# Kernel tuning notes

Hardware: AMD Instinct MI355X
Metric: run time of the kernel (lower is better)

Reference implementation:

```python
import jax, jax.numpy as jnp
import numpy as np

NUM_BITS = 4
N_VAL = 2 ** NUM_BITS - 1            # 15
INTERVAL = 2.0 / N_VAL               # init_range / n_val (non-trainable)
ZERO = 0.0                           # self.zero (non-trainable, default init)
EPS = 1e-3


def setup_inputs() -> dict:
    key = jax.random.key(0)
    k1, k2 = jax.random.split(key)
    x = jax.random.normal(k1, (32, 256, 56, 56), dtype=jnp.float32)
    # learned bin widths, initialized near `interval` with some spread
    a = (INTERVAL * (0.8 + 0.4 * jax.random.uniform(k2, (N_VAL,)))).astype(jnp.float32)
    start = jnp.full((1,), -1.0, dtype=jnp.float32)  # quantization range start
    scale1 = jnp.ones((1,), dtype=jnp.float32)
    scale2 = jnp.ones((1,), dtype=jnp.float32)
    return {"x": x, "start": start, "a": a, "scale1": scale1, "scale2": scale2}


def reference(x, start, a, scale1, scale2):
    xs = x * scale1                              # broadcast scalar
    s = start[0]
    a_pos = jnp.where(a > EPS, a, EPS)           # [n_val]
    cums = jnp.cumsum(a_pos)                     # [n_val]
    # thre_backward[i] = start + sum_{j<i} a_pos[j]
    tb = s + jnp.concatenate([jnp.zeros((1,), a_pos.dtype), cums[:-1]])
    # thre_forward[i] = thre_backward[i] + a_pos[i]/2
    tf = tb + a_pos * 0.5
    dt = xs.dtype

    # forward (hard) branch: count of strict exceedances of the sorted tf
    cnt_f = jnp.searchsorted(tf, xs, side="left")        # in [0, n_val]
    x_forward = ZERO + cnt_f.astype(dt) * jnp.asarray(INTERVAL, dt)

    # backward (soft) branch: piecewise-linear interpolation within the active bin
    cnt_b = jnp.searchsorted(tb, xs, side="left")        # in [0, n_val]
    idx = jnp.clip(cnt_b - 1, 0, N_VAL - 1)
    lin = (INTERVAL / a_pos[idx]) * (xs - tb[idx]) + ZERO + idx.astype(dt) * INTERVAL
    x_backward = jnp.where(cnt_b == 0, jnp.asarray(ZERO, dt), lin)
    top = s + cums[-1]                                    # last thre_backward + a_pos[-1]
    x_backward = jnp.where(xs > top, jnp.asarray(2.0, dt), x_backward)

    # straight-through combine: value from x_forward, gradient from x_backward
    out = jax.lax.stop_gradient(x_forward) + x_backward - jax.lax.stop_gradient(x_backward)
    return out * scale2
```

## Files before the change

kernel.cpp:

```cpp
#include <hip/hip_runtime.h>

#define NVAL 15
#define TPB  256
#define VPT  4

typedef float fvec4 __attribute__((ext_vector_type(4)));

__device__ __forceinline__ fvec4 quant4(fvec4 v, const float* tf, float sc1, float k)
{
    float xs0 = v.x * sc1, xs1 = v.y * sc1, xs2 = v.z * sc1, xs3 = v.w * sc1;
    int c0 = 0, c1 = 0, c2 = 0, c3 = 0;
#pragma unroll
    for (int i = 0; i < NVAL; ++i) {
        float t = tf[i];
        c0 += (xs0 > t);
        c1 += (xs1 > t);
        c2 += (xs2 > t);
        c3 += (xs3 > t);
    }
    fvec4 r;
    r.x = k * (float)c0;
    r.y = k * (float)c1;
    r.z = k * (float)c2;
    r.w = k * (float)c3;
    return r;
}

__global__ __launch_bounds__(TPB) void ltq_main(
    const float* __restrict__ x,
    const float* __restrict__ start,
    const float* __restrict__ a,
    const float* __restrict__ scale1,
    const float* __restrict__ scale2,
    float* __restrict__ out)
{
    const long long base = (long long)blockIdx.x * (TPB * VPT) + threadIdx.x;
    const fvec4* __restrict__ x4 = (const fvec4*)x + base;
    fvec4* __restrict__ o4 = (fvec4*)out + base;

    fvec4 v[VPT];
#pragma unroll
    for (int j = 0; j < VPT; ++j)
        v[j] = __builtin_nontemporal_load(&x4[j * TPB]);

    __builtin_amdgcn_sched_barrier(0);

    const float s   = start[0];
    const float sc1 = scale1[0];
    const float k   = (float)(2.0 / 15.0) * scale2[0];
    float tf[NVAL];
    float cum = 0.0f;
#pragma unroll
    for (int i = 0; i < NVAL; ++i) {
        float ai = a[i];
        float ap = (ai > 1e-3f) ? ai : 1e-3f;
        tf[i] = (s + cum) + 0.5f * ap;
        cum += ap;
    }

#pragma unroll
    for (int j = 0; j < VPT; ++j) {
        fvec4 r = quant4(v[j], tf, sc1, k);
        o4[j * TPB] = r;
    }
}

__global__ __launch_bounds__(TPB) void ltq_tail(
    const float* __restrict__ x,
    const float* __restrict__ start,
    const float* __restrict__ a,
    const float* __restrict__ scale1,
    const float* __restrict__ scale2,
    float* __restrict__ out,
    long long f4_done, long long n4, long long n)
{
    const float s   = start[0];
    const float sc1 = scale1[0];
    const float k   = (float)(2.0 / 15.0) * scale2[0];
    float tf[NVAL];
    float cum = 0.0f;
#pragma unroll
    for (int i = 0; i < NVAL; ++i) {
        float ai = a[i];
        float ap = (ai > 1e-3f) ? ai : 1e-3f;
        tf[i] = (s + cum) + 0.5f * ap;
        cum += ap;
    }

    const long long stride = (long long)gridDim.x * blockDim.x;
    const fvec4* __restrict__ x4 = (const fvec4*)x;
    fvec4* __restrict__ o4 = (fvec4*)out;
    for (long long i = f4_done + blockIdx.x * (long long)blockDim.x + threadIdx.x;
         i < n4; i += stride) {
        o4[i] = quant4(x4[i], tf, sc1, k);
    }
    for (long long i = (n4 << 2) + blockIdx.x * (long long)blockDim.x + threadIdx.x;
         i < n; i += stride) {
        float xs = x[i] * sc1;
        int c = 0;
#pragma unroll
        for (int t = 0; t < NVAL; ++t) c += (xs > tf[t]);
        out[i] = k * (float)c;
    }
}

extern "C" void kernel_launch(void* const* d_in, const int* in_sizes, int n_in,
                              void* d_out, int out_size, void* d_ws, size_t ws_size,
                              hipStream_t stream) {
    const float* x      = (const float*)d_in[0];
    const float* start  = (const float*)d_in[1];
    const float* a      = (const float*)d_in[2];
    const float* scale1 = (const float*)d_in[3];
    const float* scale2 = (const float*)d_in[4];
    float* out = (float*)d_out;

    const long long n  = in_sizes[0];
    const long long n4 = n >> 2;
    const long long per_block = (long long)TPB * VPT;
    const long long blocks = n4 / per_block;

    if (blocks > 0) {
        ltq_main<<<(int)blocks, TPB, 0, stream>>>(x, start, a, scale1, scale2, out);
    }
    const long long f4_done = blocks * per_block;
    if (f4_done < n4 || (n & 3)) {
        ltq_tail<<<512, TPB, 0, stream>>>(x, start, a, scale1, scale2, out,
                                          f4_done, n4, n);
    }
}
```

Baseline: 178.1 us.

## Switch main kernel to persistent grid-stride loop with fixed block count

Replaces the one-block-per-4096-vec4 launch with a fixed grid of 1792 blocks that each loop over the data in a grid-stride pattern, processing two vec4 per iteration. This amortizes the per-block threshold setup (loading a[], computing cumulative thresholds) across many elements and cuts block launch overhead. It gives up the four independent loads issued up front before compute, so fewer bytes are in flight per thread, which may reduce memory-level parallelism.

Measured after the change: 182.8 us. +2.7%, slower.

```diff
diff --git a/kernel.cpp b/kernel.cpp
--- a/kernel.cpp
+++ b/kernel.cpp
@@ -2,7 +2,6 @@
 
 #define NVAL 15
 #define TPB  256
-#define VPT  4
 
 typedef float fvec4 __attribute__((ext_vector_type(4)));
 
@@ -32,18 +31,13 @@
     const float* __restrict__ a,
     const float* __restrict__ scale1,
     const float* __restrict__ scale2,
-    float* __restrict__ out)
+    float* __restrict__ out,
+    int niter)
 {
-    const long long base = (long long)blockIdx.x * (TPB * VPT) + threadIdx.x;
-    const fvec4* __restrict__ x4 = (const fvec4*)x + base;
-    fvec4* __restrict__ o4 = (fvec4*)out + base;
-
-    fvec4 v[VPT];
-#pragma unroll
-    for (int j = 0; j < VPT; ++j)
-        v[j] = __builtin_nontemporal_load(&x4[j * TPB]);
-
-    __builtin_amdgcn_sched_barrier(0);
+    const long long tid = (long long)blockIdx.x * TPB + threadIdx.x;
+    const long long S   = (long long)gridDim.x * TPB;
+    const fvec4* __restrict__ x4 = (const fvec4*)x + tid;
+    fvec4* __restrict__ o4 = (fvec4*)out + tid;
 
     const float s   = start[0];
     const float sc1 = scale1[0];
@@ -58,10 +52,18 @@
         cum += ap;
     }
 
-#pragma unroll
-    for (int j = 0; j < VPT; ++j) {
-        fvec4 r = quant4(v[j], tf, sc1, k);
-        o4[j * TPB] = r;
+    long long off = 0;
+    int j = 0;
+    for (; j + 2 <= niter; j += 2) {
+        fvec4 v0 = __builtin_nontemporal_load(&x4[off]);
+        fvec4 v1 = __builtin_nontemporal_load(&x4[off + S]);
+        o4[off]     = quant4(v0, tf, sc1, k);
+        o4[off + S] = quant4(v1, tf, sc1, k);
+        off += 2 * S;
+    }
+    if (j < niter) {
+        fvec4 v0 = __builtin_nontemporal_load(&x4[off]);
+        o4[off] = quant4(v0, tf, sc1, k);
     }
 }
 
@@ -116,13 +118,16 @@
 
     const long long n  = in_sizes[0];
     const long long n4 = n >> 2;
-    const long long per_block = (long long)TPB * VPT;
-    const long long blocks = n4 / per_block;
 
-    if (blocks > 0) {
-        ltq_main<<<(int)blocks, TPB, 0, stream>>>(x, start, a, scale1, scale2, out);
+    const int  blocks   = 1792;
+    const long long thr = (long long)blocks * TPB;
+    const long long niter = n4 / thr;
+
+    if (niter > 0) {
+        ltq_main<<<blocks, TPB, 0, stream>>>(x, start, a, scale1, scale2, out,
+                                             (int)niter);
     }
-    const long long f4_done = blocks * per_block;
+    const long long f4_done = niter * thr;
     if (f4_done < n4 || (n & 3)) {
         ltq_tail<<<512, TPB, 0, stream>>>(x, start, a, scale1, scale2, out,
                                           f4_done, n4, n);
```
